# Kernel tuning notes

Hardware: AMD Instinct MI355X
Metric: run time of the kernel (lower is better)

The kernel has to match this reference:

```python
import jax, jax.numpy as jnp
import numpy as np

H, HD, D = 16, 64, 1024
SCALE = HD ** -0.5
TEMP = 1.0
EPS = 1e-5

def setup_inputs() -> dict:
    key = jax.random.key(0)
    ks = jax.random.split(key, 10)
    B, N = 2, 2048
    lim = 1.0 / np.sqrt(D)
    def lin(k, out_d, in_d):
        k1, k2 = jax.random.split(k)
        W = jax.random.uniform(k1, (out_d, in_d), jnp.float32, -lim, lim)
        b = jax.random.uniform(k2, (out_d,), jnp.float32, -lim, lim)
        return W, b
    Wq, bq = lin(ks[0], H * HD, D)
    Wk, bk = lin(ks[1], H * HD, D)
    Wv, bv = lin(ks[2], H * HD, D)
    Wo, bo = lin(ks[3], D, H * HD)
    return {
        "x": jax.random.normal(ks[4], (B, N, D), jnp.float32),
        "adaptive_scale": jnp.ones((H,), jnp.float32),
        "Wq": Wq, "bq": bq, "Wk": Wk, "bk": bk, "Wv": Wv, "bv": bv,
        "Wo": Wo, "bo": bo,
        "gamma": jnp.ones((D,), jnp.float32),
        "beta": jnp.zeros((D,), jnp.float32),
    }

def reference(x, adaptive_scale, Wq, bq, Wk, bk, Wv, bv, Wo, bo, gamma, beta):
    B, N, _ = x.shape
    # self-attention: context = x
    Q = (x @ Wq.T + bq).reshape(B, N, H, HD)
    K = (x @ Wk.T + bk).reshape(B, N, H, HD)
    V = (x @ Wv.T + bv).reshape(B, N, H, HD)
    # per-head adaptive scale folded into scores (matches naive QK^T * scale / temp)
    scores = jnp.einsum('bnhd,bmhd->bhnm', Q, K)
    scores = scores * (SCALE * adaptive_scale)[None, :, None, None] / TEMP
    w = jax.nn.softmax(scores, axis=-1)  # [B,H,N,N]
    attn = jnp.einsum('bhnm,bmhd->bnhd', w, V).reshape(B, N, H * HD)
    y = x + (attn @ Wo.T + bo)
    mu = jnp.mean(y, axis=-1, keepdims=True)
    var = jnp.var(y, axis=-1, keepdims=True)
    return (y - mu) / jnp.sqrt(var + EPS) * gamma + beta
```

## Files before the change

### kernel.cpp

```cpp
#include <hip/hip_runtime.h>
#include <hip/hip_bf16.h>

using bf16 = __hip_bfloat16;
typedef __attribute__((ext_vector_type(8))) short short8;
typedef __attribute__((ext_vector_type(4))) short short4v;
typedef __attribute__((ext_vector_type(4))) float f32x4;

#define MFMA16(a, b, c) __builtin_amdgcn_mfma_f32_16x16x32_bf16((a), (b), (c), 0, 0, 0)

__device__ inline void async16(bf16* lds, const bf16* g) {
  __builtin_amdgcn_global_load_lds(
      (const __attribute__((address_space(1))) void*)g,
      (__attribute__((address_space(3))) void*)lds, 16, 0, 0);
}

__device__ inline short bfs(float x) {
  union { bf16 h; short s; } u; u.h = __float2bfloat16(x); return u.s;
}
__device__ inline short4v pack4(float a, float b, float c, float d) {
  short4v r; r[0] = bfs(a); r[1] = bfs(b); r[2] = bfs(c); r[3] = bfs(d); return r;
}
__device__ inline unsigned pkt2(float x, float y) {
  return __builtin_amdgcn_perm(__float_as_uint(y), __float_as_uint(x), 0x07060302u);
}
__device__ inline float ex2(float x) {
  float r; asm("v_exp_f32 %0, %1" : "=v"(r) : "v"(x)); return r;
}
__device__ inline void pl32swap(unsigned& a, unsigned& b) {
  asm("v_permlane32_swap_b32 %0, %1" : "+v"(a), "+v"(b));
}
__device__ inline void pl16swap(unsigned& a, unsigned& b) {
  asm("v_permlane16_swap_b32 %0, %1" : "+v"(a), "+v"(b));
}

__global__ __launch_bounds__(256) void cvt_all(
    const float* __restrict__ x,  const float* __restrict__ Wq,
    const float* __restrict__ Wk, const float* __restrict__ Wv,
    const float* __restrict__ Wo,
    bf16* __restrict__ xb, bf16* __restrict__ Wqb, bf16* __restrict__ Wkb,
    bf16* __restrict__ Wvb, bf16* __restrict__ Wob) {
  int i = blockIdx.x * 256 + threadIdx.x;
  const float* s; bf16* d; int off;
  if (i < 1048576)      { s = x;  d = xb;  off = i; }
  else if (i < 1310720) { s = Wq; d = Wqb; off = i - 1048576; }
  else if (i < 1572864) { s = Wk; d = Wkb; off = i - 1310720; }
  else if (i < 1835008) { s = Wv; d = Wvb; off = i - 1572864; }
  else                  { s = Wo; d = Wob; off = i - 1835008; }
  float4 v = ((const float4*)s)[off];
  short4v o = pack4(v.x, v.y, v.z, v.w);
  *(short4v*)&d[(size_t)off * 4] = o;
}

__global__ __launch_bounds__(256) void gemm_qkv(
    const bf16* __restrict__ A,
    const bf16* __restrict__ Wq, const bf16* __restrict__ Wk, const bf16* __restrict__ Wv,
    const float* __restrict__ bq, const float* __restrict__ bk, const float* __restrict__ bv,
    const float* __restrict__ asc,
    bf16* __restrict__ Qb, bf16* __restrict__ Kb, bf16* __restrict__ Vtb) {
  __shared__ __align__(16) bf16 As[128 * 64];
  __shared__ __align__(16) bf16 Bs[64 * 64];
  __shared__ __align__(16) bf16 scrT[4][16 * 72];

  const int tid = threadIdx.x;
  const int lane = tid & 63;
  const int w = tid >> 6;
  const int m0 = blockIdx.x * 128;
  const int region = blockIdx.y >> 4;
  const int n0loc = (blockIdx.y & 15) * 64;
  const int wm = (w >> 1) * 64;
  const int wn = (w & 1) * 32;
  const int rq = lane & 15;
  const int quad = lane >> 4;

  const bf16* W = region == 0 ? Wq : (region == 1 ? Wk : Wv);
  const float* bias = region == 0 ? bq : (region == 1 ? bk : bv);
  bf16* C = region == 0 ? Qb : (region == 1 ? Kb : Vtb);

  f32x4 acc[4][2] = {};
  const bf16* Ag = A + (size_t)m0 * 1024;
  const bf16* Wg = W + (size_t)n0loc * 1024;

  const int srow = lane >> 3;
  const int sws = ((lane & 7) ^ srow) * 8;
  const int c0 = (quad ^ (rq & 7)) * 8;

  for (int k0 = 0; k0 < 1024; k0 += 64) {
    __syncthreads();
#pragma unroll
    for (int t = 0; t < 4; ++t) {
      int rb = w * 32 + t * 8;
      int row = rb + srow;
      async16(&As[rb * 64 + lane * 8], Ag + (size_t)row * 1024 + k0 + sws);
    }
#pragma unroll
    for (int t = 0; t < 2; ++t) {
      int rb = w * 16 + t * 8;
      int row = rb + srow;
      async16(&Bs[rb * 64 + lane * 8], Wg + (size_t)row * 1024 + k0 + sws);
    }
    __syncthreads();

#pragma unroll
    for (int ks = 0; ks < 2; ++ks) {
      int off = c0 ^ (ks * 32);
      short8 a[4], b[2];
#pragma unroll
      for (int i = 0; i < 4; ++i) a[i] = *(const short8*)&As[(wm + i * 16 + rq) * 64 + off];
#pragma unroll
      for (int j = 0; j < 2; ++j) b[j] = *(const short8*)&Bs[(wn + j * 16 + rq) * 64 + off];
#pragma unroll
      for (int i = 0; i < 4; ++i)
#pragma unroll
        for (int j = 0; j < 2; ++j) acc[i][j] = MFMA16(a[i], b[j], acc[i][j]);
    }
  }

  const float LOG2E = 1.44269504088896f;
  if (region < 2) {
#pragma unroll
    for (int i = 0; i < 4; ++i)
#pragma unroll
      for (int j = 0; j < 2; ++j)
#pragma unroll
        for (int r2 = 0; r2 < 4; ++r2) {
          int m = m0 + wm + i * 16 + quad * 4 + r2;
          int nr = n0loc + wn + j * 16 + rq;
          int bb = m >> 11, t = m & 2047, h = nr >> 6, hd = nr & 63;
          float v = acc[i][j][r2] + bias[nr];
          if (region == 0) v *= 0.125f * asc[h] * LOG2E;
          C[(((size_t)(bb * 16 + h)) * 2048 + t) * 64 + hd] = __float2bfloat16(v);
        }
  } else {
    const int bb = m0 >> 11;
    const int h = n0loc >> 6;
    const int tbase = (m0 & 2047) + wm;
    bf16* scr = scrT[w];
#pragma unroll
    for (int j = 0; j < 2; ++j) {
      int nr = n0loc + wn + j * 16 + rq;
      float bi = bias[nr];
#pragma unroll
      for (int i = 0; i < 4; ++i) {
        short4v pv = pack4(acc[i][j][0] + bi, acc[i][j][1] + bi,
                           acc[i][j][2] + bi, acc[i][j][3] + bi);
        *(short4v*)&scr[rq * 72 + i * 16 + quad * 4] = pv;
      }
#pragma unroll
      for (int pp = 0; pp < 4; ++pp) {
        int hdl = pp * 4 + quad;
        short4v v4 = *(const short4v*)&scr[hdl * 72 + rq * 4];
        size_t addr = (((size_t)(bb * 16 + h)) * 64 + wn + j * 16 + hdl) * 2048 + tbase + rq * 4;
        *(short4v*)&C[addr] = v4;
      }
    }
  }
}

__global__ __launch_bounds__(256) void gemm_out(
    const bf16* __restrict__ A, const bf16* __restrict__ W,
    const float* __restrict__ bias, const float* __restrict__ R,
    float* __restrict__ Y) {
  __shared__ __align__(16) bf16 As[64 * 64];
  __shared__ __align__(16) bf16 Bs[128 * 64];

  const int tid = threadIdx.x;
  const int lane = tid & 63;
  const int w = tid >> 6;
  const int m0 = blockIdx.x * 64;
  const int n0 = blockIdx.y * 128;
  const int wm = (w >> 1) * 32;
  const int wn = (w & 1) * 64;
  const int rq = lane & 15;
  const int quad = lane >> 4;

  f32x4 acc[2][4] = {};
  const bf16* Ag = A + (size_t)m0 * 1024;
  const bf16* Wg = W + (size_t)n0 * 1024;

  const int srow = lane >> 3;
  const int sws = ((lane & 7) ^ srow) * 8;
  const int c0 = (quad ^ (rq & 7)) * 8;

  for (int k0 = 0; k0 < 1024; k0 += 64) {
    __syncthreads();
#pragma unroll
    for (int t = 0; t < 2; ++t) {
      int rb = w * 16 + t * 8;
      int row = rb + srow;
      async16(&As[rb * 64 + lane * 8], Ag + (size_t)row * 1024 + k0 + sws);
    }
#pragma unroll
    for (int t = 0; t < 4; ++t) {
      int rb = w * 32 + t * 8;
      int row = rb + srow;
      async16(&Bs[rb * 64 + lane * 8], Wg + (size_t)row * 1024 + k0 + sws);
    }
    __syncthreads();

#pragma unroll
    for (int ks = 0; ks < 2; ++ks) {
      int off = c0 ^ (ks * 32);
      short8 a[2], b[4];
#pragma unroll
      for (int i = 0; i < 2; ++i) a[i] = *(const short8*)&As[(wm + i * 16 + rq) * 64 + off];
#pragma unroll
      for (int j = 0; j < 4; ++j) b[j] = *(const short8*)&Bs[(wn + j * 16 + rq) * 64 + off];
#pragma unroll
      for (int i = 0; i < 2; ++i)
#pragma unroll
        for (int j = 0; j < 4; ++j) acc[i][j] = MFMA16(a[i], b[j], acc[i][j]);
    }
  }

#pragma unroll
  for (int i = 0; i < 2; ++i)
#pragma unroll
    for (int j = 0; j < 4; ++j)
#pragma unroll
      for (int r2 = 0; r2 < 4; ++r2) {
        int m = m0 + wm + i * 16 + quad * 4 + r2;
        int n = n0 + wn + j * 16 + rq;
        Y[(size_t)m * 1024 + n] = acc[i][j][r2] + bias[n] + R[(size_t)m * 1024 + n];
      }
}

__global__ __launch_bounds__(256, 4) void attn_kernel(
    const bf16* __restrict__ Qb, const bf16* __restrict__ Kb,
    const bf16* __restrict__ Vtb,
    bf16* __restrict__ P0, bf16* __restrict__ P1, float* __restrict__ lbuf) {
  __shared__ __align__(16) bf16 Ks[64 * 64];
  __shared__ __align__(16) bf16 Vs[64 * 64];

  const int wid = blockIdx.x + (blockIdx.y << 4) + (blockIdx.z << 8);
  const int sid = (wid & 7) * 128 + (wid >> 3);
  const int q0 = (sid & 15) * 128;
  const int h = (sid >> 4) & 15;
  const int zz = sid >> 8;
  const int b = zz & 1;
  const int half = zz >> 1;

  const int tid = threadIdx.x;
  const int lane = tid & 63;
  const int w = tid >> 6;
  const int rq = lane & 15;
  const int quad = lane >> 4;

  const size_t head = ((size_t)(b * 16 + h)) * 2048 * 64;
  const bf16* Qh = Qb + head;
  const bf16* Kh = Kb + head;
  const bf16* Vh = Vtb + head;

  short8 aq[2][2];
#pragma unroll
  for (int s = 0; s < 2; ++s) {
    const bf16* qrow = Qh + (size_t)(q0 + w * 32 + s * 16 + rq) * 64;
    aq[s][0] = *(const short8*)&qrow[quad * 8];
    aq[s][1] = *(const short8*)&qrow[quad * 8 + 32];
  }

  short8 ones;
#pragma unroll
  for (int i = 0; i < 8; ++i) ones[i] = (short)0x3F80;

  const int srow = lane >> 3;
  const int swsV = ((lane & 7) ^ srow) * 8;
  const int c0 = (quad ^ (rq & 7)) * 8;
  const int c1 = c0 ^ 32;
  const int kc0 = (quad ^ (rq >> 1)) * 8;
  const int kc1 = kc0 ^ 32;

  f32x4 accO[2][4] = {};
  f32x4 lacc[2] = {};

  const int kt0 = half * 16;
  for (int kt = kt0; kt < kt0 + 16; ++kt) {
    __syncthreads();
#pragma unroll
    for (int t = 0; t < 2; ++t) {
      int rb = w * 16 + t * 8;
      int row = rb + srow;
      int swsK = ((lane & 7) ^ ((row >> 1) & 7)) * 8;
      async16(&Ks[rb * 64 + lane * 8], Kh + (size_t)(kt * 64 + row) * 64 + swsK);
      async16(&Vs[rb * 64 + lane * 8], Vh + (size_t)row * 2048 + kt * 64 + swsV);
    }
    __syncthreads();

    f32x4 S[2][4] = {};
    __builtin_amdgcn_s_setprio(1);
#pragma unroll
    for (int c = 0; c < 4; ++c) {
      const bf16* kr = &Ks[(c * 16 + rq) * 64];
      short8 k0 = *(const short8*)&kr[kc0];
      short8 k1 = *(const short8*)&kr[kc1];
      S[0][c] = MFMA16(k0, aq[0][0], S[0][c]);
      S[0][c] = MFMA16(k1, aq[0][1], S[0][c]);
      S[1][c] = MFMA16(k0, aq[1][0], S[1][c]);
      S[1][c] = MFMA16(k1, aq[1][1], S[1][c]);
    }
    __builtin_amdgcn_s_setprio(0);

    unsigned W[2][8];
#pragma unroll
    for (int s = 0; s < 2; ++s)
#pragma unroll
      for (int c = 0; c < 4; ++c) {
        W[s][c * 2 + 0] = pkt2(ex2(S[s][c][0]), ex2(S[s][c][1]));
        W[s][c * 2 + 1] = pkt2(ex2(S[s][c][2]), ex2(S[s][c][3]));
      }

    short8 ap[2][2];
#pragma unroll
    for (int s = 0; s < 2; ++s) {
      pl32swap(W[s][0], W[s][2]); pl32swap(W[s][1], W[s][3]);
      pl32swap(W[s][4], W[s][6]); pl32swap(W[s][5], W[s][7]);
      pl16swap(W[s][0], W[s][2]); pl16swap(W[s][1], W[s][3]);
      pl16swap(W[s][4], W[s][6]); pl16swap(W[s][5], W[s][7]);
      union { unsigned u[4]; short8 v; } f0, f1;
      f0.u[0] = W[s][0]; f0.u[1] = W[s][1]; f0.u[2] = W[s][2]; f0.u[3] = W[s][3];
      f1.u[0] = W[s][4]; f1.u[1] = W[s][5]; f1.u[2] = W[s][6]; f1.u[3] = W[s][7];
      ap[s][0] = f0.v; ap[s][1] = f1.v;
    }

    __builtin_amdgcn_s_setprio(1);
#pragma unroll
    for (int dt = 0; dt < 4; ++dt) {
      const bf16* vr = &Vs[(dt * 16 + rq) * 64];
      short8 v0 = *(const short8*)&vr[c0];
      short8 v1 = *(const short8*)&vr[c1];
      accO[0][dt] = MFMA16(ap[0][0], v0, accO[0][dt]);
      accO[0][dt] = MFMA16(ap[0][1], v1, accO[0][dt]);
      accO[1][dt] = MFMA16(ap[1][0], v0, accO[1][dt]);
      accO[1][dt] = MFMA16(ap[1][1], v1, accO[1][dt]);
    }
#pragma unroll
    for (int s = 0; s < 2; ++s) {
      lacc[s] = MFMA16(ap[s][0], ones, lacc[s]);
      lacc[s] = MFMA16(ap[s][1], ones, lacc[s]);
    }
    __builtin_amdgcn_s_setprio(0);
  }

  bf16* Pout = half ? P1 : P0;
  float* lout = lbuf + half * 65536;
#pragma unroll
  for (int s = 0; s < 2; ++s) {
#pragma unroll
    for (int dt = 0; dt < 4; ++dt)
#pragma unroll
      for (int r = 0; r < 4; ++r) {
        int t = q0 + w * 32 + s * 16 + quad * 4 + r;
        int d = dt * 16 + rq;
        Pout[((size_t)(b * 2048 + t)) * 1024 + h * 64 + d] =
            __float2bfloat16(accO[s][dt][r]);
      }
    if (rq == 0) {
#pragma unroll
      for (int r = 0; r < 4; ++r) {
        int t = q0 + w * 32 + s * 16 + quad * 4 + r;
        lout[(b * 16 + h) * 2048 + t] = lacc[s][r];
      }
    }
  }
}

__global__ __launch_bounds__(256) void combine_kernel(
    bf16* __restrict__ P0, const bf16* __restrict__ P1,
    const float* __restrict__ lbuf) {
  const int row = blockIdx.x;
  const int tid = threadIdx.x;
  const int col = tid * 4;
  const int b = row >> 11, t = row & 2047;
  const int h = col >> 6;
  const float l = lbuf[(b * 16 + h) * 2048 + t] + lbuf[65536 + (b * 16 + h) * 2048 + t];
  const float rl = 1.f / l;
  size_t base = (size_t)row * 1024 + col;
  short4v p0 = *(const short4v*)&P0[base];
  short4v p1 = *(const short4v*)&P1[base];
  union { short s; bf16 h; } u;
  float v[4];
#pragma unroll
  for (int i = 0; i < 4; ++i) {
    u.s = p0[i]; float a = __bfloat162float(u.h);
    u.s = p1[i]; float c = __bfloat162float(u.h);
    v[i] = (a + c) * rl;
  }
  *(short4v*)&P0[base] = pack4(v[0], v[1], v[2], v[3]);
}

__global__ __launch_bounds__(256) void ln_kernel(
    const float* __restrict__ Y, const float* __restrict__ gamma,
    const float* __restrict__ beta, float* __restrict__ out) {
  const int row = blockIdx.x;
  const int tid = threadIdx.x;
  const int lane = tid & 63;
  const int w = tid >> 6;
  const float* y = Y + (size_t)row * 1024;

  float4 v = *(const float4*)&y[tid * 4];
  float s = v.x + v.y + v.z + v.w;
  float ss = v.x * v.x + v.y * v.y + v.z * v.z + v.w * v.w;
#pragma unroll
  for (int msk = 1; msk < 64; msk <<= 1) {
    s += __shfl_xor(s, msk);
    ss += __shfl_xor(ss, msk);
  }
  __shared__ float red[2][4];
  if (lane == 0) { red[0][w] = s; red[1][w] = ss; }
  __syncthreads();
  s = red[0][0] + red[0][1] + red[0][2] + red[0][3];
  ss = red[1][0] + red[1][1] + red[1][2] + red[1][3];
  float mean = s * (1.f / 1024.f);
  float var = ss * (1.f / 1024.f) - mean * mean;
  float rstd = rsqrtf(var + 1e-5f);
  float4 g = *(const float4*)&gamma[tid * 4];
  float4 bt = *(const float4*)&beta[tid * 4];
  float4 o;
  o.x = (v.x - mean) * rstd * g.x + bt.x;
  o.y = (v.y - mean) * rstd * g.y + bt.y;
  o.z = (v.z - mean) * rstd * g.z + bt.z;
  o.w = (v.w - mean) * rstd * g.w + bt.w;
  *(float4*)&out[(size_t)row * 1024 + tid * 4] = o;
}

extern "C" void kernel_launch(void* const* d_in, const int* in_sizes, int n_in,
                              void* d_out, int out_size, void* d_ws, size_t ws_size,
                              hipStream_t stream) {
  const float* x     = (const float*)d_in[0];
  const float* asc   = (const float*)d_in[1];
  const float* Wq    = (const float*)d_in[2];
  const float* bq    = (const float*)d_in[3];
  const float* Wk    = (const float*)d_in[4];
  const float* bk    = (const float*)d_in[5];
  const float* Wv    = (const float*)d_in[6];
  const float* bv    = (const float*)d_in[7];
  const float* Wo    = (const float*)d_in[8];
  const float* bo    = (const float*)d_in[9];
  const float* gamma = (const float*)d_in[10];
  const float* beta  = (const float*)d_in[11];
  float* out = (float*)d_out;

  char* ws = (char*)d_ws;
  const size_t MB = 1024 * 1024;
  bf16* Qb   = (bf16*)(ws);
  bf16* Kb   = (bf16*)(ws + 8 * MB);
  bf16* Vtb  = (bf16*)(ws + 16 * MB);
  bf16* attn = (bf16*)(ws + 24 * MB);
  bf16* xb   = (bf16*)(ws + 32 * MB);
  bf16* Wqb  = (bf16*)(ws + 40 * MB);
  bf16* Wkb  = (bf16*)(ws + 42 * MB);
  bf16* Wvb  = (bf16*)(ws + 44 * MB);
  bf16* Wob  = (bf16*)(ws + 46 * MB);
  float* y   = (float*)(ws);
  bf16* P1   = xb;
  float* lbuf = (float*)Wqb;

  cvt_all<<<dim3(8192), dim3(256), 0, stream>>>(x, Wq, Wk, Wv, Wo, xb, Wqb, Wkb, Wvb, Wob);
  gemm_qkv<<<dim3(32, 48), dim3(256), 0, stream>>>(xb, Wqb, Wkb, Wvb, bq, bk, bv, asc, Qb, Kb, Vtb);
  attn_kernel<<<dim3(16, 16, 4), dim3(256), 0, stream>>>(Qb, Kb, Vtb, attn, P1, lbuf);
  combine_kernel<<<dim3(4096), dim3(256), 0, stream>>>(attn, P1, lbuf);
  gemm_out<<<dim3(64, 8), dim3(256), 0, stream>>>(attn, Wob, bo, x, y);
  ln_kernel<<<dim3(4096), dim3(256), 0, stream>>>(y, gamma, beta, out);
}
```

Measured before the change: 203.1 us.

## Use 8 waves per attention block and smaller output GEMM tiles

```diff
diff --git a/kernel.cpp b/kernel.cpp
--- a/kernel.cpp
+++ b/kernel.cpp
@@ -161,19 +161,19 @@
     const float* __restrict__ bias, const float* __restrict__ R,
     float* __restrict__ Y) {
   __shared__ __align__(16) bf16 As[64 * 64];
-  __shared__ __align__(16) bf16 Bs[128 * 64];
+  __shared__ __align__(16) bf16 Bs[64 * 64];
 
   const int tid = threadIdx.x;
   const int lane = tid & 63;
   const int w = tid >> 6;
   const int m0 = blockIdx.x * 64;
-  const int n0 = blockIdx.y * 128;
+  const int n0 = blockIdx.y * 64;
   const int wm = (w >> 1) * 32;
-  const int wn = (w & 1) * 64;
+  const int wn = (w & 1) * 32;
   const int rq = lane & 15;
   const int quad = lane >> 4;
 
-  f32x4 acc[2][4] = {};
+  f32x4 acc[2][2] = {};
   const bf16* Ag = A + (size_t)m0 * 1024;
   const bf16* Wg = W + (size_t)n0 * 1024;
 
@@ -188,11 +188,6 @@
       int rb = w * 16 + t * 8;
       int row = rb + srow;
       async16(&As[rb * 64 + lane * 8], Ag + (size_t)row * 1024 + k0 + sws);
-    }
-#pragma unroll
-    for (int t = 0; t < 4; ++t) {
-      int rb = w * 32 + t * 8;
-      int row = rb + srow;
       async16(&Bs[rb * 64 + lane * 8], Wg + (size_t)row * 1024 + k0 + sws);
     }
     __syncthreads();
@@ -200,22 +195,22 @@
 #pragma unroll
     for (int ks = 0; ks < 2; ++ks) {
       int off = c0 ^ (ks * 32);
-      short8 a[2], b[4];
+      short8 a[2], b[2];
 #pragma unroll
       for (int i = 0; i < 2; ++i) a[i] = *(const short8*)&As[(wm + i * 16 + rq) * 64 + off];
 #pragma unroll
-      for (int j = 0; j < 4; ++j) b[j] = *(const short8*)&Bs[(wn + j * 16 + rq) * 64 + off];
+      for (int j = 0; j < 2; ++j) b[j] = *(const short8*)&Bs[(wn + j * 16 + rq) * 64 + off];
 #pragma unroll
       for (int i = 0; i < 2; ++i)
 #pragma unroll
-        for (int j = 0; j < 4; ++j) acc[i][j] = MFMA16(a[i], b[j], acc[i][j]);
+        for (int j = 0; j < 2; ++j) acc[i][j] = MFMA16(a[i], b[j], acc[i][j]);
     }
   }
 
 #pragma unroll
   for (int i = 0; i < 2; ++i)
 #pragma unroll
-    for (int j = 0; j < 4; ++j)
+    for (int j = 0; j < 2; ++j)
 #pragma unroll
       for (int r2 = 0; r2 < 4; ++r2) {
         int m = m0 + wm + i * 16 + quad * 4 + r2;
@@ -224,7 +219,7 @@
       }
 }
 
-__global__ __launch_bounds__(256, 4) void attn_kernel(
+__global__ __launch_bounds__(512, 6) void attn_kernel(
     const bf16* __restrict__ Qb, const bf16* __restrict__ Kb,
     const bf16* __restrict__ Vtb,
     bf16* __restrict__ P0, bf16* __restrict__ P1, float* __restrict__ lbuf) {
@@ -250,12 +245,11 @@
   const bf16* Kh = Kb + head;
   const bf16* Vh = Vtb + head;
 
-  short8 aq[2][2];
-#pragma unroll
-  for (int s = 0; s < 2; ++s) {
-    const bf16* qrow = Qh + (size_t)(q0 + w * 32 + s * 16 + rq) * 64;
-    aq[s][0] = *(const short8*)&qrow[quad * 8];
-    aq[s][1] = *(const short8*)&qrow[quad * 8 + 32];
+  short8 aq0, aq1;
+  {
+    const bf16* qrow = Qh + (size_t)(q0 + w * 16 + rq) * 64;
+    aq0 = *(const short8*)&qrow[quad * 8];
+    aq1 = *(const short8*)&qrow[quad * 8 + 32];
   }
 
   short8 ones;
@@ -269,15 +263,14 @@
   const int kc0 = (quad ^ (rq >> 1)) * 8;
   const int kc1 = kc0 ^ 32;
 
-  f32x4 accO[2][4] = {};
-  f32x4 lacc[2] = {};
+  f32x4 accO[4] = {};
+  f32x4 lacc = {};
 
   const int kt0 = half * 16;
   for (int kt = kt0; kt < kt0 + 16; ++kt) {
     __syncthreads();
-#pragma unroll
-    for (int t = 0; t < 2; ++t) {
-      int rb = w * 16 + t * 8;
+    {
+      int rb = w * 8;
       int row = rb + srow;
       int swsK = ((lane & 7) ^ ((row >> 1) & 7)) * 8;
       async16(&Ks[rb * 64 + lane * 8], Kh + (size_t)(kt * 64 + row) * 64 + swsK);
@@ -285,40 +278,35 @@
     }
     __syncthreads();
 
-    f32x4 S[2][4] = {};
+    f32x4 S[4] = {};
     __builtin_amdgcn_s_setprio(1);
 #pragma unroll
     for (int c = 0; c < 4; ++c) {
       const bf16* kr = &Ks[(c * 16 + rq) * 64];
       short8 k0 = *(const short8*)&kr[kc0];
       short8 k1 = *(const short8*)&kr[kc1];
-      S[0][c] = MFMA16(k0, aq[0][0], S[0][c]);
-      S[0][c] = MFMA16(k1, aq[0][1], S[0][c]);
-      S[1][c] = MFMA16(k0, aq[1][0], S[1][c]);
-      S[1][c] = MFMA16(k1, aq[1][1], S[1][c]);
+      S[c] = MFMA16(k0, aq0, S[c]);
+      S[c] = MFMA16(k1, aq1, S[c]);
     }
     __builtin_amdgcn_s_setprio(0);
 
-    unsigned W[2][8];
-#pragma unroll
-    for (int s = 0; s < 2; ++s)
-#pragma unroll
-      for (int c = 0; c < 4; ++c) {
-        W[s][c * 2 + 0] = pkt2(ex2(S[s][c][0]), ex2(S[s][c][1]));
-        W[s][c * 2 + 1] = pkt2(ex2(S[s][c][2]), ex2(S[s][c][3]));
-      }
-
-    short8 ap[2][2];
-#pragma unroll
-    for (int s = 0; s < 2; ++s) {
-      pl32swap(W[s][0], W[s][2]); pl32swap(W[s][1], W[s][3]);
-      pl32swap(W[s][4], W[s][6]); pl32swap(W[s][5], W[s][7]);
-      pl16swap(W[s][0], W[s][2]); pl16swap(W[s][1], W[s][3]);
-      pl16swap(W[s][4], W[s][6]); pl16swap(W[s][5], W[s][7]);
+    unsigned W[8];
+#pragma unroll
+    for (int c = 0; c < 4; ++c) {
+      W[c * 2 + 0] = pkt2(ex2(S[c][0]), ex2(S[c][1]));
+      W[c * 2 + 1] = pkt2(ex2(S[c][2]), ex2(S[c][3]));
+    }
+
+    short8 ap0, ap1;
+    {
+      pl32swap(W[0], W[2]); pl32swap(W[1], W[3]);
+      pl32swap(W[4], W[6]); pl32swap(W[5], W[7]);
+      pl16swap(W[0], W[2]); pl16swap(W[1], W[3]);
+      pl16swap(W[4], W[6]); pl16swap(W[5], W[7]);
       union { unsigned u[4]; short8 v; } f0, f1;
-      f0.u[0] = W[s][0]; f0.u[1] = W[s][1]; f0.u[2] = W[s][2]; f0.u[3] = W[s][3];
-      f1.u[0] = W[s][4]; f1.u[1] = W[s][5]; f1.u[2] = W[s][6]; f1.u[3] = W[s][7];
-      ap[s][0] = f0.v; ap[s][1] = f1.v;
+      f0.u[0] = W[0]; f0.u[1] = W[1]; f0.u[2] = W[2]; f0.u[3] = W[3];
+      f1.u[0] = W[4]; f1.u[1] = W[5]; f1.u[2] = W[6]; f1.u[3] = W[7];
+      ap0 = f0.v; ap1 = f1.v;
     }
 
     __builtin_amdgcn_s_setprio(1);
@@ -327,38 +315,30 @@
       const bf16* vr = &Vs[(dt * 16 + rq) * 64];
       short8 v0 = *(const short8*)&vr[c0];
       short8 v1 = *(const short8*)&vr[c1];
-      accO[0][dt] = MFMA16(ap[0][0], v0, accO[0][dt]);
-      accO[0][dt] = MFMA16(ap[0][1], v1, accO[0][dt]);
-      accO[1][dt] = MFMA16(ap[1][0], v0, accO[1][dt]);
-      accO[1][dt] = MFMA16(ap[1][1], v1, accO[1][dt]);
-    }
-#pragma unroll
-    for (int s = 0; s < 2; ++s) {
-      lacc[s] = MFMA16(ap[s][0], ones, lacc[s]);
-      lacc[s] = MFMA16(ap[s][1], ones, lacc[s]);
-    }
+      accO[dt] = MFMA16(ap0, v0, accO[dt]);
+      accO[dt] = MFMA16(ap1, v1, accO[dt]);
+    }
+    lacc = MFMA16(ap0, ones, lacc);
+    lacc = MFMA16(ap1, ones, lacc);
     __builtin_amdgcn_s_setprio(0);
   }
 
   bf16* Pout = half ? P1 : P0;
   float* lout = lbuf + half * 65536;
 #pragma unroll
-  for (int s = 0; s < 2; ++s) {
-#pragma unroll
-    for (int dt = 0; dt < 4; ++dt)
-#pragma unroll
-      for (int r = 0; r < 4; ++r) {
-        int t = q0 + w * 32 + s * 16 + quad * 4 + r;
-        int d = dt * 16 + rq;
-        Pout[((size_t)(b * 2048 + t)) * 1024 + h * 64 + d] =
-            __float2bfloat16(accO[s][dt][r]);
-      }
-    if (rq == 0) {
-#pragma unroll
-      for (int r = 0; r < 4; ++r) {
-        int t = q0 + w * 32 + s * 16 + quad * 4 + r;
-        lout[(b * 16 + h) * 2048 + t] = lacc[s][r];
-      }
+  for (int dt = 0; dt < 4; ++dt)
+#pragma unroll
+    for (int r = 0; r < 4; ++r) {
+      int t = q0 + w * 16 + quad * 4 + r;
+      int d = dt * 16 + rq;
+      Pout[((size_t)(b * 2048 + t)) * 1024 + h * 64 + d] =
+          __float2bfloat16(accO[dt][r]);
+    }
+  if (rq == 0) {
+#pragma unroll
+    for (int r = 0; r < 4; ++r) {
+      int t = q0 + w * 16 + quad * 4 + r;
+      lout[(b * 16 + h) * 2048 + t] = lacc[r];
     }
   }
 }
@@ -456,8 +436,8 @@
 
   cvt_all<<<dim3(8192), dim3(256), 0, stream>>>(x, Wq, Wk, Wv, Wo, xb, Wqb, Wkb, Wvb, Wob);
   gemm_qkv<<<dim3(32, 48), dim3(256), 0, stream>>>(xb, Wqb, Wkb, Wvb, bq, bk, bv, asc, Qb, Kb, Vtb);
-  attn_kernel<<<dim3(16, 16, 4), dim3(256), 0, stream>>>(Qb, Kb, Vtb, attn, P1, lbuf);
+  attn_kernel<<<dim3(16, 16, 4), dim3(512), 0, stream>>>(Qb, Kb, Vtb, attn, P1, lbuf);
   combine_kernel<<<dim3(4096), dim3(256), 0, stream>>>(attn, P1, lbuf);
-  gemm_out<<<dim3(64, 8), dim3(256), 0, stream>>>(attn, Wob, bo, x, y);
+  gemm_out<<<dim3(64, 16), dim3(256), 0, stream>>>(attn, Wob, bo, x, y);
   ln_kernel<<<dim3(4096), dim3(256), 0, stream>>>(y, gamma, beta, out);
 }
```

Measured after the change: 204.1 us. Within noise of the previous version (+0.4%).
